# Kernel optimization log

Hardware: AMD Instinct MI355X
Metric: run time of the kernel (lower is better)

Reference implementation:

```python
import jax, jax.numpy as jnp
import numpy as np


def fwht(x):
    """Fast Walsh-Hadamard transform over the last dim (power of 2), normalized by 1/sqrt(n)."""
    n = x.shape[-1]
    orig_shape = x.shape
    x = x.reshape(-1, n)
    h = 1
    while h < n:
        x = x.reshape(-1, n // (2 * h), 2, h)
        a = x[:, :, 0, :]
        b = x[:, :, 1, :]
        x = jnp.stack([a + b, a - b], axis=2)
        h *= 2
    x = x.reshape(orig_shape)
    return x * (1.0 / jnp.sqrt(jnp.asarray(n, dtype=x.dtype)))


def act_quant(x, bits):
    """Per-token absmax symmetric quantization with straight-through estimator."""
    qb = 2.0 ** (bits - 1) - 1.0  # 127 for 8 bits
    scale = qb / jnp.clip(jnp.max(jnp.abs(x), axis=-1, keepdims=True), 1e-5, None)
    q = jnp.clip(jnp.round(x * scale), -qb, qb) / scale
    return x + jax.lax.stop_gradient(q - x)


def weight_quant(w):
    """BitNet b1.58 ternary weight quantization (per-tensor mean-abs scale) with STE."""
    scale = jnp.clip(jnp.mean(jnp.abs(w)), 1e-5, None)
    q = jnp.clip(jnp.round(w / scale), -1.0, 1.0) * scale
    return w + jax.lax.stop_gradient(q - w)


def hbitlinear(x, w, bits):
    # Hadamard rotate activations, quantize acts + ternary weights, then GEMM.
    xh = fwht(x)
    xq = act_quant(xh, bits)
    wq = weight_quant(w)
    return jnp.einsum('bsh,oh->bso', xq, wq)


def setup_inputs() -> dict:
    key = jax.random.key(0)
    k1, k2, k3 = jax.random.split(key, 3)
    B, S, H = 4, 2048, 2048
    I = 4096  # intermediate = hidden * mlp_ratio(2.0)
    hidden_states = jax.random.normal(k1, (B, S, H), dtype=jnp.float32)
    w_up = jax.random.normal(k2, (I, H), dtype=jnp.float32) * 0.02
    w_down = jax.random.normal(k3, (H, I), dtype=jnp.float32) * 0.02
    return {"hidden_states": hidden_states, "w_up": w_up, "w_down": w_down}


def reference(hidden_states, w_up, w_down):
    ACT_BITS = 8
    h = hbitlinear(hidden_states, w_up, ACT_BITS)   # (B, S, I)
    h = jnp.square(jax.nn.relu(h))                  # ReLU^2
    # dropout with p=0.0 (eval/identity)
    out = hbitlinear(h, w_down, ACT_BITS)           # (B, S, H)
    return out
```

## Files before the change

### kernel.cpp

```cpp
#include <hip/hip_runtime.h>
#include <hip/hip_bf16.h>
#include <hip/hip_fp16.h>

typedef int i32x4 __attribute__((ext_vector_type(4)));

#define GLL16(g, l) __builtin_amdgcn_global_load_lds( \
    (const __attribute__((address_space(1))) void*)(g), \
    (__attribute__((address_space(3))) void*)(l), 16, 0, 0)

#define CFENCE() asm volatile("" ::: "memory")

__global__ __launch_bounds__(256) void abs_sum2_kernel(const float* __restrict__ w0,
                                                       const float* __restrict__ w1, int n4,
                                                       double* __restrict__ out)
{
    const int sel = blockIdx.x & 1;
    const float4* w4 = (const float4*)(sel ? w1 : w0);
    const int b = blockIdx.x >> 1, nb = gridDim.x >> 1;
    double acc = 0.0;
    for (int i = b * blockDim.x + threadIdx.x; i < n4; i += nb * blockDim.x) {
        float4 v = w4[i];
        acc += (double)fabsf(v.x) + (double)fabsf(v.y) + (double)fabsf(v.z) + (double)fabsf(v.w);
    }
    for (int o = 32; o > 0; o >>= 1) acc += __shfl_down(acc, o, 64);
    __shared__ double part[4];
    int lane = threadIdx.x & 63, wv = threadIdx.x >> 6;
    if (lane == 0) part[wv] = acc;
    __syncthreads();
    if (threadIdx.x == 0) atomicAdd(&out[sel], part[0] + part[1] + part[2] + part[3]);
}

__global__ __launch_bounds__(256) void wquant2_kernel(const float* __restrict__ w0,
                                                      const float* __restrict__ w1, int n4,
                                                      const double* __restrict__ sums, double inv_count,
                                                      char* __restrict__ o0, char* __restrict__ o1)
{
    const int sel = blockIdx.x & 1;
    const float4* w4 = (const float4*)(sel ? w1 : w0);
    char4* o4 = (char4*)(sel ? o1 : o0);
    float s = (float)(sums[sel] * inv_count);
    s = fmaxf(s, 1e-5f);
    const float t0 = 0.5f * s;
    const int b = blockIdx.x >> 1, nb = gridDim.x >> 1;
    for (int i = b * blockDim.x + threadIdx.x; i < n4; i += nb * blockDim.x) {
        float4 v = w4[i];
        char4 c;
        c.x = (fabsf(v.x) > t0) ? (v.x > 0.0f ? 1 : -1) : 0;
        c.y = (fabsf(v.y) > t0) ? (v.y > 0.0f ? 1 : -1) : 0;
        c.z = (fabsf(v.z) > t0) ? (v.z > 0.0f ? 1 : -1) : 0;
        c.w = (fabsf(v.w) > t0) ? (v.w > 0.0f ? 1 : -1) : 0;
        o4[i] = c;
    }
}

template<int NS>
__device__ __forceinline__ void hreg(float* v)
{
    #pragma unroll
    for (int h = 1; h < (1 << NS); h <<= 1)
        #pragma unroll
        for (int i = 0; i < 16; i++)
            if ((i & h) == 0) { float a = v[i], b = v[i + h]; v[i] = a + b; v[i + h] = a - b; }
}

__device__ __forceinline__ int lswz(int e)
{
    const int r16 = e >> 4;
    return r16 * 16 + 4 * (((e >> 2) & 3) ^ ((r16 >> 1) & 3)) + (e & 3);
}

template<int N, int TOKS>
__global__ __launch_bounds__(256) void fwht_quant_kernel(
    const float* __restrict__ in, long in_stride,
    char* __restrict__ outq, long out_stride,
    float* __restrict__ scales)
{
    constexpr int L = 256 / TOKS;
    static_assert(N == 16 * L, "N must be 16*threads-per-token");
    __shared__ float sx[TOKS * N];
    __shared__ float red[4];

    const int tid = threadIdx.x;
    const int tk  = tid / L;
    const int lt  = tid % L;
    const long tok = (long)blockIdx.x * TOKS + tk;
    const float* row = in + tok * in_stride;
    float* s = sx + tk * N;

    float v[16];
    {
        const float4* r4 = (const float4*)(row + (size_t)lt * 16);
        float4 a[4];
        #pragma unroll
        for (int i = 0; i < 4; i++) a[i] = r4[i];
        #pragma unroll
        for (int i = 0; i < 4; i++) {
            v[4*i] = a[i].x; v[4*i+1] = a[i].y; v[4*i+2] = a[i].z; v[4*i+3] = a[i].w;
        }
    }
    hreg<4>(v);
    {
        const int psw = (lt >> 1) & 3;
        #pragma unroll
        for (int i = 0; i < 4; i++)
            *(float4*)(s + lt * 16 + 4 * (i ^ psw)) =
                make_float4(v[4*i], v[4*i+1], v[4*i+2], v[4*i+3]);
    }
    __syncthreads();

    const int o = lt & 15, ss = lt >> 4;
    #pragma unroll
    for (int j = 0; j < 16; j++) v[j] = s[lswz(o + 256 * ss + 16 * j)];
    hreg<(L == 256) ? 4 : 3>(v);
    #pragma unroll
    for (int j = 0; j < 16; j++) s[lswz(o + 256 * ss + 16 * j)] = v[j];
    __syncthreads();

    #pragma unroll
    for (int j = 0; j < 16; j++) v[j] = s[lswz(o + 16 * ss + L * j)];
    hreg<4>(v);

    const float rn = 1.0f / sqrtf((float)N);
    float m = 0.0f;
    #pragma unroll
    for (int j = 0; j < 16; j++) { v[j] *= rn; m = fmaxf(m, fabsf(v[j])); }
    for (int off = 32; off > 0; off >>= 1) m = fmaxf(m, __shfl_down(m, off, 64));
    if ((tid & 63) == 0) red[tid >> 6] = m;
    __syncthreads();
    float mm;
    if (TOKS == 1) mm = fmaxf(fmaxf(red[0], red[1]), fmaxf(red[2], red[3]));
    else           mm = fmaxf(red[2 * tk], red[2 * tk + 1]);
    mm = fmaxf(mm, 1e-5f);
    const float sc = 127.0f / mm;
    if (lt == 0) scales[tok] = sc;
    __syncthreads();

    char* ct = (char*)sx + tk * N;
    #pragma unroll
    for (int j = 0; j < 16; j++) {
        float q = fminf(fmaxf(rintf(v[j] * sc), -127.0f), 127.0f);
        ct[o + 16 * ss + L * j] = (char)q;
    }
    __syncthreads();
    int4* dst = (int4*)(outq + tok * out_stride);
    dst[lt] = ((const int4*)ct)[lt];
}

__global__ __launch_bounds__(256) void fwht_quant_f16_kernel(
    const __half* __restrict__ in, long in_stride,
    char* __restrict__ outq, long out_stride,
    float* __restrict__ scales)
{
    constexpr int N = 4096, L = 256;
    __shared__ float sx[N];
    __shared__ float red[4];

    const int lt = threadIdx.x;
    const long tok = blockIdx.x;
    const __half* row = in + tok * in_stride;
    float* s = sx;

    float v[16];
    {
        const int4* r4 = (const int4*)row;
        int4 q0 = r4[2 * lt], q1 = r4[2 * lt + 1];
        const __half2* h0 = (const __half2*)&q0;
        const __half2* h1 = (const __half2*)&q1;
        #pragma unroll
        for (int i = 0; i < 4; i++) {
            float2 f = __half22float2(h0[i]);
            v[2*i] = f.x; v[2*i+1] = f.y;
        }
        #pragma unroll
        for (int i = 0; i < 4; i++) {
            float2 f = __half22float2(h1[i]);
            v[8+2*i] = f.x; v[8+2*i+1] = f.y;
        }
    }
    hreg<4>(v);
    {
        const int psw = (lt >> 1) & 3;
        #pragma unroll
        for (int i = 0; i < 4; i++)
            *(float4*)(s + lt * 16 + 4 * (i ^ psw)) =
                make_float4(v[4*i], v[4*i+1], v[4*i+2], v[4*i+3]);
    }
    __syncthreads();

    const int o = lt & 15, ss = lt >> 4;
    #pragma unroll
    for (int j = 0; j < 16; j++) v[j] = s[lswz(o + 256 * ss + 16 * j)];
    hreg<4>(v);
    #pragma unroll
    for (int j = 0; j < 16; j++) s[lswz(o + 256 * ss + 16 * j)] = v[j];
    __syncthreads();

    #pragma unroll
    for (int j = 0; j < 16; j++) v[j] = s[lswz(o + 16 * ss + L * j)];
    hreg<4>(v);

    const float rn = 1.0f / sqrtf((float)N);
    float m = 0.0f;
    #pragma unroll
    for (int j = 0; j < 16; j++) { v[j] *= rn; m = fmaxf(m, fabsf(v[j])); }
    for (int off = 32; off > 0; off >>= 1) m = fmaxf(m, __shfl_down(m, off, 64));
    if ((lt & 63) == 0) red[lt >> 6] = m;
    __syncthreads();
    float mm = fmaxf(fmaxf(red[0], red[1]), fmaxf(red[2], red[3]));
    mm = fmaxf(mm, 1e-5f);
    const float sc = 127.0f / mm;
    if (lt == 0) scales[tok] = sc;
    __syncthreads();

    char* ct = (char*)sx;
    #pragma unroll
    for (int j = 0; j < 16; j++) {
        float q = fminf(fmaxf(rintf(v[j] * sc), -127.0f), 127.0f);
        ct[o + 16 * ss + L * j] = (char)q;
    }
    __syncthreads();
    int4* dst = (int4*)(outq + tok * out_stride);
    dst[lt] = ((const int4*)ct)[lt];
}

#define BM 128
#define BN 128
#define BK 64

__global__ __launch_bounds__(256, 3) void gemm_bt_kernel(
    const char* __restrict__ A, int lda,
    const char* __restrict__ B, int ldb,
    void* __restrict__ Cv, int ldc,
    int K, int lognx,
    const float* __restrict__ sx,
    const double* __restrict__ wsum, double inv_count,
    int do_relu2, int out_f16)
{
    __shared__ __align__(16) char As[2][BM * BK];
    __shared__ __align__(16) char Bs[2][BN * BK];

    const int bid = blockIdx.x;
    const int xcd = bid & 7;
    const int n = bid >> 3;
    const int nper = gridDim.x >> 3;
    const int bx = n & ((1 << lognx) - 1);
    const int by = xcd * (nper >> lognx) + (n >> lognx);
    const int row0 = by * BM;
    const int col0 = bx * BN;

    const int tid = threadIdx.x;
    const int lane = tid & 63;
    const int w = tid >> 6;
    const int wr = w >> 1;
    const int wc = w & 1;

    i32x4 acc[4][4] = {};

    const int srow = w * 16 + (lane >> 2);
    const int sseg = ((lane & 3) ^ ((lane >> 3) & 3)) << 4;
    const char* Ag0 = A + (size_t)(row0 + srow) * lda + sseg;
    const char* Ag1 = Ag0 + (size_t)64 * lda;
    const char* Bg0 = B + (size_t)(col0 + srow) * ldb + sseg;
    const char* Bg1 = Bg0 + (size_t)64 * ldb;
    const int wdst = w * 1024;

    const int fr = lane & 15;
    const int fks = lane >> 4;
    const int rsw = ((fks ^ ((fr >> 1) & 3)) << 4);
    const int aoff = (wr * 64 + fr) * BK + rsw;
    const int boff = (wc * 64 + fr) * BK + rsw;

    const int NT = K >> 6;

    auto stage = [&](int tt) {
        const int sb = tt & 1;
        const int ko = tt * BK;
        GLL16(Ag0 + ko, &As[sb][wdst]);
        GLL16(Ag1 + ko, &As[sb][wdst + 4096]);
        GLL16(Bg0 + ko, &Bs[sb][wdst]);
        GLL16(Bg1 + ko, &Bs[sb][wdst + 4096]);
    };
    auto compute = [&](int t) __attribute__((always_inline)) {
        const char* as = As[t & 1];
        const char* bs = Bs[t & 1];
        i32x4 af[4], bf[4];
        #pragma unroll
        for (int i = 0; i < 4; ++i) af[i] = *(const i32x4*)(as + aoff + i * 1024);
        #pragma unroll
        for (int j = 0; j < 4; ++j) bf[j] = *(const i32x4*)(bs + boff + j * 1024);
        __builtin_amdgcn_s_setprio(1);
        #pragma unroll
        for (int i = 0; i < 4; ++i)
            #pragma unroll
            for (int j = 0; j < 4; ++j)
                acc[i][j] = __builtin_amdgcn_mfma_i32_16x16x64_i8(af[i], bf[j], acc[i][j], 0, 0, 0);
        __builtin_amdgcn_s_setprio(0);
    };

    stage(0);
    asm volatile("s_waitcnt vmcnt(0)" ::: "memory");
    __builtin_amdgcn_s_barrier();
    CFENCE();

    for (int t = 0; t < NT - 1; ++t) {
        stage(t + 1);
        compute(t);
        asm volatile("s_waitcnt vmcnt(0)" ::: "memory");
        __builtin_amdgcn_s_barrier();
        CFENCE();
    }
    compute(NT - 1);

    float sw = (float)(wsum[0] * inv_count);
    sw = fmaxf(sw, 1e-5f);
    const int qd = lane >> 4;
    if (out_f16) {
        __half* C = (__half*)Cv;
        #pragma unroll
        for (int i = 0; i < 4; ++i) {
            #pragma unroll
            for (int r = 0; r < 4; ++r) {
                int rowm = row0 + wr * 64 + i * 16 + qd * 4 + r;
                float esc = sw / sx[rowm];
                __half* crow = C + (size_t)rowm * ldc + col0 + wc * 64;
                #pragma unroll
                for (int j = 0; j < 4; ++j) {
                    float v = (float)acc[i][j][r] * esc;
                    if (do_relu2) { v = fmaxf(v, 0.0f); v = v * v; }
                    crow[j * 16 + fr] = __float2half(v);
                }
            }
        }
    } else {
        float* C = (float*)Cv;
        #pragma unroll
        for (int i = 0; i < 4; ++i) {
            #pragma unroll
            for (int r = 0; r < 4; ++r) {
                int rowm = row0 + wr * 64 + i * 16 + qd * 4 + r;
                float esc = sw / sx[rowm];
                float* crow = C + (size_t)rowm * ldc + col0 + wc * 64;
                #pragma unroll
                for (int j = 0; j < 4; ++j) {
                    float v = (float)acc[i][j][r] * esc;
                    if (do_relu2) { v = fmaxf(v, 0.0f); v = v * v; }
                    crow[j * 16 + fr] = v;
                }
            }
        }
    }
}

extern "C" void kernel_launch(void* const* d_in, const int* in_sizes, int n_in,
                              void* d_out, int out_size, void* d_ws, size_t ws_size,
                              hipStream_t stream)
{
    const float* X   = (const float*)d_in[0];
    const float* Wup = (const float*)d_in[1];
    const float* Wdn = (const float*)d_in[2];
    float* out = (float*)d_out;

    const int Mtok = 8192, H = 2048, I = 4096;
    const int NW = H * I;

    char* ws = (char*)d_ws;
    double* sums = (double*)ws;
    float* sx1 = (float*)(ws + 1024);
    float* sx2 = (float*)(ws + 1024 + 32768);
    char* wqup = ws + (1 << 20);
    char* wqdn = wqup + (size_t)NW;
    char* xq1  = wqdn + (size_t)NW;
    char* hbuf = xq1 + (size_t)Mtok * H;

    hipMemsetAsync(sums, 0, 16, stream);
    abs_sum2_kernel<<<1024, 256, 0, stream>>>(Wup, Wdn, NW / 4, sums);
    const double invc = 1.0 / (double)NW;
    wquant2_kernel<<<2048, 256, 0, stream>>>(Wup, Wdn, NW / 4, sums, invc, wqup, wqdn);

    fwht_quant_kernel<2048, 2><<<Mtok / 2, 256, 0, stream>>>(X, H, xq1, H, sx1);
    gemm_bt_kernel<<<(I / BN) * (Mtok / BM), 256, 0, stream>>>(
        xq1, H, wqup, H, hbuf, I, H, 5, sx1, &sums[0], invc, 1, 1);
    fwht_quant_f16_kernel<<<Mtok, 256, 0, stream>>>((const __half*)hbuf, I, hbuf, 2 * I, sx2);
    gemm_bt_kernel<<<(H / BN) * (Mtok / BM), 256, 0, stream>>>(
        (const char*)hbuf, 2 * I, wqdn, I, out, H, I, 4, sx2, &sums[1], invc, 0, 0);
}
```

Before: 362.4 us.

## Pre-pack ternary weights into MFMA fragment order and load B directly to registers

Weight quantization now writes int8 weights in the per-lane MFMA fragment layout, so the GEMM loads B operands straight from global memory into registers and no longer stages them through LDS. The GEMM loop is unrolled by two with double-buffered B register sets and a relaxed vmcnt wait. The activation FWHT-quant and the weight abs-sum are fused into one launch to cut a kernel launch. This halves LDS traffic and use per block but relies on L2/global latency for B fragments and adds register pressure under the 3-blocks-per-SM bound.

```diff
diff --git a/kernel.cpp b/kernel.cpp
--- a/kernel.cpp
+++ b/kernel.cpp
@@ -10,49 +10,6 @@
 
 #define CFENCE() asm volatile("" ::: "memory")
 
-__global__ __launch_bounds__(256) void abs_sum2_kernel(const float* __restrict__ w0,
-                                                       const float* __restrict__ w1, int n4,
-                                                       double* __restrict__ out)
-{
-    const int sel = blockIdx.x & 1;
-    const float4* w4 = (const float4*)(sel ? w1 : w0);
-    const int b = blockIdx.x >> 1, nb = gridDim.x >> 1;
-    double acc = 0.0;
-    for (int i = b * blockDim.x + threadIdx.x; i < n4; i += nb * blockDim.x) {
-        float4 v = w4[i];
-        acc += (double)fabsf(v.x) + (double)fabsf(v.y) + (double)fabsf(v.z) + (double)fabsf(v.w);
-    }
-    for (int o = 32; o > 0; o >>= 1) acc += __shfl_down(acc, o, 64);
-    __shared__ double part[4];
-    int lane = threadIdx.x & 63, wv = threadIdx.x >> 6;
-    if (lane == 0) part[wv] = acc;
-    __syncthreads();
-    if (threadIdx.x == 0) atomicAdd(&out[sel], part[0] + part[1] + part[2] + part[3]);
-}
-
-__global__ __launch_bounds__(256) void wquant2_kernel(const float* __restrict__ w0,
-                                                      const float* __restrict__ w1, int n4,
-                                                      const double* __restrict__ sums, double inv_count,
-                                                      char* __restrict__ o0, char* __restrict__ o1)
-{
-    const int sel = blockIdx.x & 1;
-    const float4* w4 = (const float4*)(sel ? w1 : w0);
-    char4* o4 = (char4*)(sel ? o1 : o0);
-    float s = (float)(sums[sel] * inv_count);
-    s = fmaxf(s, 1e-5f);
-    const float t0 = 0.5f * s;
-    const int b = blockIdx.x >> 1, nb = gridDim.x >> 1;
-    for (int i = b * blockDim.x + threadIdx.x; i < n4; i += nb * blockDim.x) {
-        float4 v = w4[i];
-        char4 c;
-        c.x = (fabsf(v.x) > t0) ? (v.x > 0.0f ? 1 : -1) : 0;
-        c.y = (fabsf(v.y) > t0) ? (v.y > 0.0f ? 1 : -1) : 0;
-        c.z = (fabsf(v.z) > t0) ? (v.z > 0.0f ? 1 : -1) : 0;
-        c.w = (fabsf(v.w) > t0) ? (v.w > 0.0f ? 1 : -1) : 0;
-        o4[i] = c;
-    }
-}
-
 template<int NS>
 __device__ __forceinline__ void hreg(float* v)
 {
@@ -70,7 +27,8 @@
 }
 
 template<int N, int TOKS>
-__global__ __launch_bounds__(256) void fwht_quant_kernel(
+__device__ __forceinline__ void fwht_quant_body(
+    int bid,
     const float* __restrict__ in, long in_stride,
     char* __restrict__ outq, long out_stride,
     float* __restrict__ scales)
@@ -83,7 +41,7 @@
     const int tid = threadIdx.x;
     const int tk  = tid / L;
     const int lt  = tid % L;
-    const long tok = (long)blockIdx.x * TOKS + tk;
+    const long tok = (long)bid * TOKS + tk;
     const float* row = in + tok * in_stride;
     float* s = sx + tk * N;
 
@@ -146,6 +104,73 @@
     dst[lt] = ((const int4*)ct)[lt];
 }
 
+__device__ __forceinline__ void abs_sum_body(int bid, int nb,
+                                             const float* __restrict__ w0,
+                                             const float* __restrict__ w1, int n4,
+                                             double* __restrict__ out)
+{
+    const int sel = bid & 1;
+    const float4* w4 = (const float4*)(sel ? w1 : w0);
+    const int b = bid >> 1, nbb = nb >> 1;
+    double acc = 0.0;
+    for (int i = b * blockDim.x + threadIdx.x; i < n4; i += nbb * blockDim.x) {
+        float4 v = w4[i];
+        acc += (double)fabsf(v.x) + (double)fabsf(v.y) + (double)fabsf(v.z) + (double)fabsf(v.w);
+    }
+    for (int o = 32; o > 0; o >>= 1) acc += __shfl_down(acc, o, 64);
+    __shared__ double part[4];
+    int lane = threadIdx.x & 63, wv = threadIdx.x >> 6;
+    if (lane == 0) part[wv] = acc;
+    __syncthreads();
+    if (threadIdx.x == 0) atomicAdd(&out[sel], part[0] + part[1] + part[2] + part[3]);
+}
+
+__global__ __launch_bounds__(256) void fused_fwht_abs_kernel(
+    const float* __restrict__ X, char* __restrict__ xq1, float* __restrict__ sx1,
+    const float* __restrict__ w0, const float* __restrict__ w1, int n4,
+    double* __restrict__ sums, int nfw, int nabs)
+{
+    if ((int)blockIdx.x < nfw)
+        fwht_quant_body<2048, 2>(blockIdx.x, X, 2048, xq1, 2048, sx1);
+    else
+        abs_sum_body(blockIdx.x - nfw, nabs, w0, w1, n4, sums);
+}
+
+__global__ __launch_bounds__(256) void wquant_pack_kernel(
+    const float* __restrict__ w0, const float* __restrict__ w1,
+    const double* __restrict__ sums, double inv_count,
+    char* __restrict__ o0, char* __restrict__ o1)
+{
+    const int sel = blockIdx.x & 1;
+    const float* wp = sel ? w1 : w0;
+    char* op = sel ? o1 : o0;
+    const int K = sel ? 4096 : 2048;
+    const int kshift = sel ? 6 : 5;
+    float s = (float)(sums[sel] * inv_count);
+    s = fmaxf(s, 1e-5f);
+    const float t0 = 0.5f * s;
+
+    const int c = (int)(blockIdx.x >> 1) * 256 + threadIdx.x;
+    const int lane = c & 63;
+    const int g = c >> 6;
+    const int kt = g & ((1 << kshift) - 1);
+    const int ot = g >> kshift;
+    const int o = ot * 16 + (lane & 15);
+    const int k0 = (kt << 6) + ((lane >> 4) << 4);
+
+    const float4* r4 = (const float4*)(wp + (size_t)o * K + k0);
+    float4 a[4];
+    #pragma unroll
+    for (int i = 0; i < 4; i++) a[i] = r4[i];
+
+    union { char ch[16]; int4 v; } u;
+    const float* f = (const float*)a;
+    #pragma unroll
+    for (int i = 0; i < 16; i++)
+        u.ch[i] = (fabsf(f[i]) > t0) ? (f[i] > 0.0f ? 1 : -1) : 0;
+    *(int4*)(op + (size_t)c * 16) = u.v;
+}
+
 __global__ __launch_bounds__(256) void fwht_quant_f16_kernel(
     const __half* __restrict__ in, long in_stride,
     char* __restrict__ outq, long out_stride,
@@ -229,7 +254,7 @@
 
 __global__ __launch_bounds__(256, 3) void gemm_bt_kernel(
     const char* __restrict__ A, int lda,
-    const char* __restrict__ B, int ldb,
+    const char* __restrict__ Bp,
     void* __restrict__ Cv, int ldc,
     int K, int lognx,
     const float* __restrict__ sx,
@@ -237,7 +262,6 @@
     int do_relu2, int out_f16)
 {
     __shared__ __align__(16) char As[2][BM * BK];
-    __shared__ __align__(16) char Bs[2][BN * BK];
 
     const int bid = blockIdx.x;
     const int xcd = bid & 7;
@@ -260,15 +284,16 @@
     const int sseg = ((lane & 3) ^ ((lane >> 3) & 3)) << 4;
     const char* Ag0 = A + (size_t)(row0 + srow) * lda + sseg;
     const char* Ag1 = Ag0 + (size_t)64 * lda;
-    const char* Bg0 = B + (size_t)(col0 + srow) * ldb + sseg;
-    const char* Bg1 = Bg0 + (size_t)64 * ldb;
     const int wdst = w * 1024;
 
     const int fr = lane & 15;
     const int fks = lane >> 4;
     const int rsw = ((fks ^ ((fr >> 1) & 3)) << 4);
     const int aoff = (wr * 64 + fr) * BK + rsw;
-    const int boff = (wc * 64 + fr) * BK + rsw;
+
+    const int NKT = K >> 6;
+    const size_t jstep = (size_t)NKT << 10;
+    const char* Bb = Bp + (((size_t)((col0 >> 4) + wc * 4) * NKT) << 10) + (lane << 4);
 
     const int NT = K >> 6;
 
@@ -277,39 +302,56 @@
         const int ko = tt * BK;
         GLL16(Ag0 + ko, &As[sb][wdst]);
         GLL16(Ag1 + ko, &As[sb][wdst + 4096]);
-        GLL16(Bg0 + ko, &Bs[sb][wdst]);
-        GLL16(Bg1 + ko, &Bs[sb][wdst + 4096]);
     };
-    auto compute = [&](int t) __attribute__((always_inline)) {
+    auto bload = [&](i32x4* bq, int tt) __attribute__((always_inline)) {
+        const size_t to = (size_t)tt << 10;
+        #pragma unroll
+        for (int j = 0; j < 4; ++j) bq[j] = *(const i32x4*)(Bb + j * jstep + to);
+    };
+    auto compute = [&](int t, const i32x4* bq) __attribute__((always_inline)) {
         const char* as = As[t & 1];
-        const char* bs = Bs[t & 1];
-        i32x4 af[4], bf[4];
+        i32x4 af[4];
         #pragma unroll
         for (int i = 0; i < 4; ++i) af[i] = *(const i32x4*)(as + aoff + i * 1024);
-        #pragma unroll
-        for (int j = 0; j < 4; ++j) bf[j] = *(const i32x4*)(bs + boff + j * 1024);
         __builtin_amdgcn_s_setprio(1);
         #pragma unroll
         for (int i = 0; i < 4; ++i)
             #pragma unroll
             for (int j = 0; j < 4; ++j)
-                acc[i][j] = __builtin_amdgcn_mfma_i32_16x16x64_i8(af[i], bf[j], acc[i][j], 0, 0, 0);
+                acc[i][j] = __builtin_amdgcn_mfma_i32_16x16x64_i8(af[i], bq[j], acc[i][j], 0, 0, 0);
         __builtin_amdgcn_s_setprio(0);
     };
 
+    i32x4 bqA[4], bqB[4];
+
     stage(0);
+    bload(bqA, 0);
     asm volatile("s_waitcnt vmcnt(0)" ::: "memory");
     __builtin_amdgcn_s_barrier();
     CFENCE();
 
-    for (int t = 0; t < NT - 1; ++t) {
+    int t = 0;
+    for (; t < NT - 2; t += 2) {
         stage(t + 1);
-        compute(t);
-        asm volatile("s_waitcnt vmcnt(0)" ::: "memory");
+        bload(bqB, t + 1);
+        compute(t, bqA);
+        asm volatile("s_waitcnt vmcnt(4)" ::: "memory");
         __builtin_amdgcn_s_barrier();
         CFENCE();
-    }
-    compute(NT - 1);
+        stage(t + 2);
+        bload(bqA, t + 2);
+        compute(t + 1, bqB);
+        asm volatile("s_waitcnt vmcnt(4)" ::: "memory");
+        __builtin_amdgcn_s_barrier();
+        CFENCE();
+    }
+    stage(NT - 1);
+    bload(bqB, NT - 1);
+    compute(NT - 2, bqA);
+    asm volatile("s_waitcnt vmcnt(4)" ::: "memory");
+    __builtin_amdgcn_s_barrier();
+    CFENCE();
+    compute(NT - 1, bqB);
 
     float sw = (float)(wsum[0] * inv_count);
     sw = fmaxf(sw, 1e-5f);
@@ -373,14 +415,14 @@
     char* hbuf = xq1 + (size_t)Mtok * H;
 
     hipMemsetAsync(sums, 0, 16, stream);
-    abs_sum2_kernel<<<1024, 256, 0, stream>>>(Wup, Wdn, NW / 4, sums);
+    fused_fwht_abs_kernel<<<4096 + 1024, 256, 0, stream>>>(
+        X, xq1, sx1, Wup, Wdn, NW / 4, sums, 4096, 1024);
     const double invc = 1.0 / (double)NW;
-    wquant2_kernel<<<2048, 256, 0, stream>>>(Wup, Wdn, NW / 4, sums, invc, wqup, wqdn);
-
-    fwht_quant_kernel<2048, 2><<<Mtok / 2, 256, 0, stream>>>(X, H, xq1, H, sx1);
+    wquant_pack_kernel<<<4096, 256, 0, stream>>>(Wup, Wdn, sums, invc, wqup, wqdn);
+
     gemm_bt_kernel<<<(I / BN) * (Mtok / BM), 256, 0, stream>>>(
-        xq1, H, wqup, H, hbuf, I, H, 5, sx1, &sums[0], invc, 1, 1);
+        xq1, H, wqup, hbuf, I, H, 5, sx1, &sums[0], invc, 1, 1);
     fwht_quant_f16_kernel<<<Mtok, 256, 0, stream>>>((const __half*)hbuf, I, hbuf, 2 * I, sx2);
     gemm_bt_kernel<<<(H / BN) * (Mtok / BM), 256, 0, stream>>>(
-        (const char*)hbuf, 2 * I, wqdn, I, out, H, I, 4, sx2, &sums[1], invc, 0, 0);
-}
+        (const char*)hbuf, 2 * I, wqdn, out, H, I, 4, sx2, &sums[1], invc, 0, 0);
+}
```

New measurement: 367.7 us. No clear change (+1.5%).
